# Kernel tuning notes

Hardware: AMD Instinct MI355X
Metric: run time of the kernel (lower is better)

Reference implementation:

```python
import jax, jax.numpy as jnp
import numpy as np

DIM = 1024
LN_EPS = 1e-5


def setup_inputs() -> dict:
    key = jax.random.key(0)
    ks = jax.random.split(key, 6)
    B, S, D = 8, 2048, DIM
    x = jax.random.normal(ks[0], (B, S, D), dtype=jnp.float32)
    mask = jnp.ones((B, S, 1), dtype=jnp.float32)
    # LayerNorm params
    ln_g = jnp.ones((D,), dtype=jnp.float32)
    ln_b = jnp.zeros((D,), dtype=jnp.float32)
    # FeedForward: Linear(D, D) -> GELU -> Linear(D, D); hidden_dim == dim per source
    lim = 1.0 / np.sqrt(D)
    w1 = jax.random.uniform(ks[1], (D, D), jnp.float32, -lim, lim)
    b1 = jax.random.uniform(ks[2], (D,), jnp.float32, -lim, lim)
    w2 = jax.random.uniform(ks[3], (D, D), jnp.float32, -lim, lim)
    b2 = jax.random.uniform(ks[4], (D,), jnp.float32, -lim, lim)
    return {"x": x, "mask": mask, "ln_g": ln_g, "ln_b": ln_b,
            "w1": w1, "b1": b1, "w2": w2, "b2": b2}


def _layernorm(t, g, b):
    mu = jnp.mean(t, axis=-1, keepdims=True)
    var = jnp.mean(jnp.square(t - mu), axis=-1, keepdims=True)
    return (t - mu) * jax.lax.rsqrt(var + LN_EPS) * g + b


def reference(x, mask, ln_g, ln_b, w1, b1, w2, b2):
    # torch.fft(t, signal_ndim=1): FFT over hidden axis (complex input, imag=0)
    ft = jnp.fft.fft(x.astype(jnp.float32), axis=-1)
    # torch.fft(., signal_ndim=2): 2D FFT over (seq, hidden)
    ft = jnp.fft.fft2(ft, axes=(-2, -1))
    ft = ft.real  # [..., 0] slice of the fake-complex tensor
    t = _layernorm(x + ft, ln_g, ln_b)
    # FeedForward: Linear -> GELU(exact) -> Linear (dropout is identity at eval)
    h = jax.nn.gelu(t @ w1 + b1, approximate=False)
    out = h @ w2 + b2
    return out * mask
```

## Files before the change

### kernel.cpp

```cpp
#include <hip/hip_runtime.h>
#include <math.h>

#define DIMD 1024
#define SEQ  2048
#define BATCH 8
#define ROWS (BATCH * SEQ)

#define MF 1152
#define KF 1088

typedef __attribute__((ext_vector_type(8))) short bf16x8;
typedef __attribute__((ext_vector_type(4))) float f32x4;
typedef __attribute__((ext_vector_type(16))) float f32x16;
typedef __attribute__((ext_vector_type(8))) unsigned short ushort8;

__device__ __forceinline__ unsigned short f2bf(float f) {
    unsigned u = __float_as_uint(f);
    unsigned r = (u + 0x7FFFu + ((u >> 16) & 1u)) >> 16;
    return (unsigned short)r;
}
__device__ __forceinline__ void gl_lds16(const void* g, void* l) {
    __builtin_amdgcn_global_load_lds(
        (const __attribute__((address_space(1))) unsigned int*)g,
        (__attribute__((address_space(3))) unsigned int*)l, 16, 0, 0);
}


__global__ __launch_bounds__(256) void build_acos(unsigned short* __restrict__ Acos) {
    int s = blockIdx.x;
    for (int t = threadIdx.x; t < KF; t += 256) {
        float c = 0.0f;
        if (t <= 1024) {
            int prod = (s * t) & (SEQ - 1);
            c = 1024.0f * cospif((float)prod * (1.0f / 1024.0f));
        }
        Acos[(size_t)s * KF + t] = f2bf(c);
    }
}

__global__ __launch_bounds__(256) void build_xe(const float* __restrict__ x,
                                                unsigned short* __restrict__ Xe) {
    int lane = threadIdx.x & 63;
    int oct  = threadIdx.x >> 6;
    int n = blockIdx.x * 64 + lane;
    int b = n >> 10, d = n & 1023;
    int rd = (DIMD - d) & (DIMD - 1);
    int t0 = blockIdx.y * 32 + oct * 8;
    const float* xb = x + (size_t)b * SEQ * DIMD + rd;
    ushort8 tmp;
    #pragma unroll
    for (int j = 0; j < 8; ++j) {
        int t = t0 + j;
        float v;
        if (t == 0)          v = xb[0];
        else if (t < 1024)   v = xb[(size_t)t * DIMD] + xb[(size_t)(2048 - t) * DIMD];
        else if (t == 1024)  v = xb[(size_t)1024 * DIMD];
        else                 v = 0.0f;
        tmp[j] = f2bf(v);
    }
    *(ushort8*)&Xe[(size_t)n * KF + t0] = tmp;
}

__global__ __launch_bounds__(256) void pack_wt(const float* __restrict__ W,
                                               unsigned short* __restrict__ Wt) {
    int lane = threadIdx.x & 63;
    int oct = threadIdx.x >> 6;
    int n = blockIdx.x * 64 + lane;
    int k0 = blockIdx.y * 32 + oct * 8;
    ushort8 tmp;
    #pragma unroll
    for (int j = 0; j < 8; ++j) tmp[j] = f2bf(W[(size_t)(k0 + j) * DIMD + n]);
    *(ushort8*)&Wt[(size_t)n * DIMD + k0] = tmp;
}

template <int MODE>
__global__ __launch_bounds__(256, 2) void gemm32(const unsigned short* __restrict__ A,
                                                 const unsigned short* __restrict__ B,
                                                 int K, int lda, int ldb, int ldc,
                                                 const float* __restrict__ bias,
                                                 const float* __restrict__ mask,
                                                 void* __restrict__ outp) {
    __shared__ unsigned short As[2][128 * 64];
    __shared__ unsigned short Bs[2][128 * 64];

    const int tid  = threadIdx.x;
    const int lane = tid & 63;
    const int w    = tid >> 6;
    const int wm   = w >> 1;
    const int wn   = w & 1;
    const int r31  = lane & 31;
    const int hl   = lane >> 5;
    const int sw   = lane & 7;

    const int st_row = lane >> 3;
    const int st_col = ((lane & 7) ^ st_row) * 8;

    int bx = blockIdx.x, by = blockIdx.y;
    if (MODE != 0) {
        int lin = bx + 8 * by;
        int c = lin & 7, r = lin >> 3;
        by = c * 16 + (r >> 3);
        bx = r & 7;
    }
    const int m0 = by * 128;
    const int n0 = bx * 128;

    const int rA = wm * 64 + r31;
    const int rB = wn * 64 + r31;

    auto stage = [&](int buf, int kt) {
        int kb = kt * 64 + st_col;
        #pragma unroll
        for (int c = 0; c < 4; ++c) {
            int ch = w + c * 4;
            gl_lds16(&A[(size_t)(m0 + ch * 8 + st_row) * lda + kb], &As[buf][ch * 512]);
            gl_lds16(&B[(size_t)(n0 + ch * 8 + st_row) * ldb + kb], &Bs[buf][ch * 512]);
        }
    };

    f32x16 acc[2][2] = {};
    bf16x8 a0[2], b0[2], a1[2], b1[2];

#define READK(SA, SB, PA, PB, KK)                                                    \
    {                                                                                \
        const int so_ = ((((KK) * 2) + hl) ^ sw) * 8;                                \
        _Pragma("unroll") for (int bi = 0; bi < 2; ++bi)                             \
            SA[bi] = *(const bf16x8*)&(PA)[(rA + bi * 32) * 64 + so_];               \
        _Pragma("unroll") for (int bj = 0; bj < 2; ++bj)                             \
            SB[bj] = *(const bf16x8*)&(PB)[(rB + bj * 32) * 64 + so_];               \
    }

#define MFMAK(SA, SB)                                                                \
    __builtin_amdgcn_s_setprio(1);                                                   \
    _Pragma("unroll") for (int bi = 0; bi < 2; ++bi)                                 \
        _Pragma("unroll") for (int bj = 0; bj < 2; ++bj)                             \
            acc[bi][bj] = __builtin_amdgcn_mfma_f32_32x32x16_bf16(                   \
                SA[bi], SB[bj], acc[bi][bj], 0, 0, 0);                               \
    __builtin_amdgcn_s_setprio(0);

    const int NT = K >> 6;

    stage(0, 0);
    asm volatile("s_waitcnt vmcnt(0)" ::: "memory");
    __builtin_amdgcn_s_barrier();

    int cur = 0;
    for (int t = 0; t < NT; ++t) {
        const unsigned short* pa = &As[cur][0];
        const unsigned short* pb = &Bs[cur][0];
        int nk = (t + 1 < NT) ? t + 1 : NT - 1;
        READK(a0, b0, pa, pb, 0)
        stage(cur ^ 1, nk);
        READK(a1, b1, pa, pb, 1)
        MFMAK(a0, b0)
        READK(a0, b0, pa, pb, 2)
        MFMAK(a1, b1)
        READK(a1, b1, pa, pb, 3)
        MFMAK(a0, b0)
        MFMAK(a1, b1)
        asm volatile("s_waitcnt vmcnt(0) lgkmcnt(0)" ::: "memory");
        __builtin_amdgcn_s_barrier();
        cur ^= 1;
    }
#undef MFMAK
#undef READK

    #pragma unroll
    for (int bi = 0; bi < 2; ++bi) {
        int rowb = m0 + wm * 64 + bi * 32 + 4 * hl;
        #pragma unroll
        for (int bj = 0; bj < 2; ++bj) {
            int col = n0 + wn * 64 + bj * 32 + r31;
            float bcol = (MODE != 0) ? bias[col] : 0.0f;
            #pragma unroll
            for (int r = 0; r < 16; ++r) {
                float v = acc[bi][bj][r];
                int row = rowb + (r & 3) + 8 * (r >> 2);
                if (MODE == 0) {
                    ((float*)outp)[(size_t)row * ldc + col] = v;
                } else if (MODE == 1) {
                    v += bcol;
                    v = 0.5f * v * (1.0f + erff(v * 0.70710678118654752f));
                    ((unsigned short*)outp)[(size_t)row * ldc + col] = f2bf(v);
                } else {
                    v += bcol;
                    v *= mask[row];
                    ((float*)outp)[(size_t)row * ldc + col] = v;
                }
            }
        }
    }
}

__global__ __launch_bounds__(256) void ln_pair(const float* __restrict__ x,
                                               const float* __restrict__ F,
                                               const float* __restrict__ g,
                                               const float* __restrict__ beta,
                                               unsigned short* __restrict__ t) {
    const int sp = blockIdx.x;
    const int b  = blockIdx.y;

    float4 fv = ((const float4*)(F + (size_t)sp * 8192 + (size_t)b * 1024))[threadIdx.x];
    float4 g4 = ((const float4*)g)[threadIdx.x];
    float4 b4 = ((const float4*)beta)[threadIdx.x];

    __shared__ float red[4];
    const int wave = threadIdx.x >> 6;
    const int lane = threadIdx.x & 63;

    const int nrows = (sp >= 1 && sp <= 1023) ? 2 : 1;
    for (int p = 0; p < nrows; ++p) {
        int s = p ? (2048 - sp) : sp;
        int row = b * SEQ + s;
        float4 xv = ((const float4*)(x + (size_t)row * DIMD))[threadIdx.x];
        float v0 = xv.x + fv.x, v1 = xv.y + fv.y, v2 = xv.z + fv.z, v3 = xv.w + fv.w;

        float sm = v0 + v1 + v2 + v3;
        #pragma unroll
        for (int off = 32; off > 0; off >>= 1) sm += __shfl_down(sm, off, 64);
        if (lane == 0) red[wave] = sm;
        __syncthreads();
        const float mean = (red[0] + red[1] + red[2] + red[3]) * (1.0f / DIMD);

        float dx0 = v0 - mean, dx1 = v1 - mean, dx2 = v2 - mean, dx3 = v3 - mean;
        float q = dx0 * dx0 + dx1 * dx1 + dx2 * dx2 + dx3 * dx3;
        __syncthreads();
        #pragma unroll
        for (int off = 32; off > 0; off >>= 1) q += __shfl_down(q, off, 64);
        if (lane == 0) red[wave] = q;
        __syncthreads();
        const float var = (red[0] + red[1] + red[2] + red[3]) * (1.0f / DIMD);
        const float rstd = rsqrtf(var + 1e-5f);

        ushort4 o;
        o.x = f2bf(dx0 * rstd * g4.x + b4.x);
        o.y = f2bf(dx1 * rstd * g4.y + b4.y);
        o.z = f2bf(dx2 * rstd * g4.z + b4.z);
        o.w = f2bf(dx3 * rstd * g4.w + b4.w);
        ((ushort4*)(t + (size_t)row * DIMD))[threadIdx.x] = o;
        __syncthreads();
    }
}

#define BM 64
#define BN 64
#define BK 16

__global__ __launch_bounds__(256) void fft_cos_kernel(const float* __restrict__ x,
                                                      float* __restrict__ y) {
    __shared__ float tab[SEQ];
    __shared__ float As[BM][BK + 1];
    __shared__ float Bs[BK][BN + 1];
    const int tid = threadIdx.x;
    const int b = blockIdx.z;
    const int s0 = blockIdx.y * BM;
    const int n0 = blockIdx.x * BN;
    for (int i = tid; i < SEQ; i += 256) tab[i] = cospif((float)i * (1.0f / 1024.0f));
    const int tx = tid & 15;
    const int ty = tid >> 4;
    float acc[4][4] = {};
    const float* Xb = x + (size_t)b * SEQ * DIMD;
    for (int k0 = 0; k0 < SEQ; k0 += BK) {
        __syncthreads();
        for (int f = tid; f < BM * BK; f += 256) {
            int i = f / BK, k = f % BK;
            int prod = (s0 + i) * (k0 + k);
            As[i][k] = tab[prod & (SEQ - 1)];
        }
        for (int f = tid; f < BK * BN; f += 256) {
            int k = f / BN, j = f % BN;
            int d = n0 + j;
            int rd = (DIMD - d) & (DIMD - 1);
            Bs[k][j] = Xb[(size_t)(k0 + k) * DIMD + rd];
        }
        __syncthreads();
        #pragma unroll
        for (int k = 0; k < BK; ++k) {
            float a[4], bv[4];
            #pragma unroll
            for (int i = 0; i < 4; ++i) a[i] = As[ty * 4 + i][k];
            #pragma unroll
            for (int j = 0; j < 4; ++j) bv[j] = Bs[k][tx * 4 + j];
            #pragma unroll
            for (int i = 0; i < 4; ++i)
                #pragma unroll
                for (int j = 0; j < 4; ++j) acc[i][j] += a[i] * bv[j];
        }
    }
    #pragma unroll
    for (int i = 0; i < 4; ++i) {
        int s = s0 + ty * 4 + i;
        #pragma unroll
        for (int j = 0; j < 4; ++j) {
            int d = n0 + tx * 4 + j;
            y[((size_t)b * SEQ + s) * DIMD + d] = Xb[(size_t)s * DIMD + d] + 1024.0f * acc[i][j];
        }
    }
}

__global__ __launch_bounds__(256) void ln_kernel(float* __restrict__ y,
                                                 const float* __restrict__ g,
                                                 const float* __restrict__ beta) {
    const int row = blockIdx.x;
    float4* p = (float4*)(y + (size_t)row * DIMD);
    float4 v = p[threadIdx.x];
    __shared__ float red[4];
    const int wave = threadIdx.x >> 6;
    const int lane = threadIdx.x & 63;
    float s = v.x + v.y + v.z + v.w;
    #pragma unroll
    for (int off = 32; off > 0; off >>= 1) s += __shfl_down(s, off, 64);
    if (lane == 0) red[wave] = s;
    __syncthreads();
    const float mean = (red[0] + red[1] + red[2] + red[3]) * (1.0f / DIMD);
    float dx0 = v.x - mean, dx1 = v.y - mean, dx2 = v.z - mean, dx3 = v.w - mean;
    float q = dx0 * dx0 + dx1 * dx1 + dx2 * dx2 + dx3 * dx3;
    __syncthreads();
    #pragma unroll
    for (int off = 32; off > 0; off >>= 1) q += __shfl_down(q, off, 64);
    if (lane == 0) red[wave] = q;
    __syncthreads();
    const float var = (red[0] + red[1] + red[2] + red[3]) * (1.0f / DIMD);
    const float rstd = rsqrtf(var + 1e-5f);
    float4 g4 = ((const float4*)g)[threadIdx.x];
    float4 b4 = ((const float4*)beta)[threadIdx.x];
    float4 o;
    o.x = dx0 * rstd * g4.x + b4.x;
    o.y = dx1 * rstd * g4.y + b4.y;
    o.z = dx2 * rstd * g4.z + b4.z;
    o.w = dx3 * rstd * g4.w + b4.w;
    p[threadIdx.x] = o;
}

template <int MODE>
__global__ __launch_bounds__(256) void ff_gemm(const float* __restrict__ A,
                                               const float* __restrict__ W,
                                               const float* __restrict__ bias,
                                               const float* __restrict__ mask,
                                               float* __restrict__ out) {
    __shared__ float As[BM][BK + 1];
    __shared__ float Bs[BK][BN + 1];
    const int tid = threadIdx.x;
    const int tx = tid & 15;
    const int ty = tid >> 4;
    const int m0 = blockIdx.y * BM;
    const int n0 = blockIdx.x * BN;
    float acc[4][4] = {};
    for (int k0 = 0; k0 < DIMD; k0 += BK) {
        __syncthreads();
        for (int f = tid; f < BM * BK; f += 256) {
            int i = f / BK, k = f % BK;
            As[i][k] = A[(size_t)(m0 + i) * DIMD + k0 + k];
        }
        for (int f = tid; f < BK * BN; f += 256) {
            int k = f / BN, j = f % BN;
            Bs[k][j] = W[(size_t)(k0 + k) * DIMD + n0 + j];
        }
        __syncthreads();
        #pragma unroll
        for (int k = 0; k < BK; ++k) {
            float a[4], bv[4];
            #pragma unroll
            for (int i = 0; i < 4; ++i) a[i] = As[ty * 4 + i][k];
            #pragma unroll
            for (int j = 0; j < 4; ++j) bv[j] = Bs[k][tx * 4 + j];
            #pragma unroll
            for (int i = 0; i < 4; ++i)
                #pragma unroll
                for (int j = 0; j < 4; ++j) acc[i][j] += a[i] * bv[j];
        }
    }
    #pragma unroll
    for (int i = 0; i < 4; ++i) {
        int m = m0 + ty * 4 + i;
        float mk = (MODE == 1) ? mask[m] : 1.0f;
        #pragma unroll
        for (int j = 0; j < 4; ++j) {
            int n = n0 + tx * 4 + j;
            float v = acc[i][j] + bias[n];
            if (MODE == 0) v = 0.5f * v * (1.0f + erff(v * 0.70710678118654752f));
            else v *= mk;
            out[(size_t)m * DIMD + n] = v;
        }
    }
}

extern "C" void kernel_launch(void* const* d_in, const int* in_sizes, int n_in,
                              void* d_out, int out_size, void* d_ws, size_t ws_size,
                              hipStream_t stream) {
    const float* x    = (const float*)d_in[0];
    const float* mask = (const float*)d_in[1];
    const float* ln_g = (const float*)d_in[2];
    const float* ln_b = (const float*)d_in[3];
    const float* w1   = (const float*)d_in[4];
    const float* b1   = (const float*)d_in[5];
    const float* w2   = (const float*)d_in[6];
    const float* b2   = (const float*)d_in[7];
    float* out = (float*)d_out;

    const size_t MB = 1024 * 1024;
    dim3 blk(256);

    if (ws_size >= 70 * MB) {
        char* w = (char*)d_ws;
        unsigned short* Acos = (unsigned short*)w;
        unsigned short* Xe   = (unsigned short*)(w + 4 * MB);
        unsigned short* t    = (unsigned short*)(w + 32 * MB);
        unsigned short* h    = (unsigned short*)w;
        unsigned short* W1t  = (unsigned short*)(w + 64 * MB);
        unsigned short* W2t  = (unsigned short*)(w + 66 * MB);
        float* F = (float*)d_out;

        build_acos<<<dim3(MF), blk, 0, stream>>>(Acos);
        build_xe<<<dim3(8192 / 64, KF / 32), blk, 0, stream>>>(x, Xe);
        pack_wt<<<dim3(1024 / 64, 1024 / 32), blk, 0, stream>>>(w1, W1t);
        pack_wt<<<dim3(1024 / 64, 1024 / 32), blk, 0, stream>>>(w2, W2t);

        gemm32<0><<<dim3(8192 / 128, MF / 128), blk, 0, stream>>>(
            Acos, Xe, KF, KF, KF, 8192, nullptr, nullptr, F);
        ln_pair<<<dim3(1025, BATCH), blk, 0, stream>>>(x, F, ln_g, ln_b, t);
        gemm32<1><<<dim3(1024 / 128, ROWS / 128), blk, 0, stream>>>(
            t, W1t, 1024, 1024, 1024, 1024, b1, nullptr, h);
        gemm32<2><<<dim3(1024 / 128, ROWS / 128), blk, 0, stream>>>(
            h, W2t, 1024, 1024, 1024, 1024, b2, mask, out);
    } else {
        float* yf = (float*)d_ws;
        const size_t bufBytes = (size_t)ROWS * DIMD * sizeof(float);
        fft_cos_kernel<<<dim3(DIMD / BN, SEQ / BM, BATCH), blk, 0, stream>>>(x, yf);
        ln_kernel<<<dim3(ROWS), blk, 0, stream>>>(yf, ln_g, ln_b);
        ff_gemm<0><<<dim3(DIMD / BN, ROWS / BM), blk, 0, stream>>>(yf, w1, b1, nullptr, out);
        ff_gemm<1><<<dim3(DIMD / BN, ROWS / BM), blk, 0, stream>>>(out, w2, b2, mask, yf);
        hipMemcpyAsync(d_out, yf, bufBytes, hipMemcpyDeviceToDevice, stream);
    }
}
```

Before: 317.9 us.

## Fuse prep kernels and switch GEMMs to 128x64 single-buffered tiles

```diff
diff --git a/kernel.cpp b/kernel.cpp
--- a/kernel.cpp
+++ b/kernel.cpp
@@ -10,7 +10,6 @@
 #define KF 1088
 
 typedef __attribute__((ext_vector_type(8))) short bf16x8;
-typedef __attribute__((ext_vector_type(4))) float f32x4;
 typedef __attribute__((ext_vector_type(16))) float f32x16;
 typedef __attribute__((ext_vector_type(8))) unsigned short ushort8;
 
@@ -25,152 +24,161 @@
         (__attribute__((address_space(3))) unsigned int*)l, 16, 0, 0);
 }
 
-
-__global__ __launch_bounds__(256) void build_acos(unsigned short* __restrict__ Acos) {
-    int s = blockIdx.x;
-    for (int t = threadIdx.x; t < KF; t += 256) {
-        float c = 0.0f;
-        if (t <= 1024) {
-            int prod = (s * t) & (SEQ - 1);
-            c = 1024.0f * cospif((float)prod * (1.0f / 1024.0f));
-        }
-        Acos[(size_t)s * KF + t] = f2bf(c);
-    }
-}
-
-__global__ __launch_bounds__(256) void build_xe(const float* __restrict__ x,
-                                                unsigned short* __restrict__ Xe) {
-    int lane = threadIdx.x & 63;
-    int oct  = threadIdx.x >> 6;
-    int n = blockIdx.x * 64 + lane;
-    int b = n >> 10, d = n & 1023;
-    int rd = (DIMD - d) & (DIMD - 1);
-    int t0 = blockIdx.y * 32 + oct * 8;
-    const float* xb = x + (size_t)b * SEQ * DIMD + rd;
-    ushort8 tmp;
-    #pragma unroll
-    for (int j = 0; j < 8; ++j) {
-        int t = t0 + j;
-        float v;
-        if (t == 0)          v = xb[0];
-        else if (t < 1024)   v = xb[(size_t)t * DIMD] + xb[(size_t)(2048 - t) * DIMD];
-        else if (t == 1024)  v = xb[(size_t)1024 * DIMD];
-        else                 v = 0.0f;
-        tmp[j] = f2bf(v);
-    }
-    *(ushort8*)&Xe[(size_t)n * KF + t0] = tmp;
-}
-
-__global__ __launch_bounds__(256) void pack_wt(const float* __restrict__ W,
-                                               unsigned short* __restrict__ Wt) {
-    int lane = threadIdx.x & 63;
-    int oct = threadIdx.x >> 6;
-    int n = blockIdx.x * 64 + lane;
-    int k0 = blockIdx.y * 32 + oct * 8;
-    ushort8 tmp;
-    #pragma unroll
-    for (int j = 0; j < 8; ++j) tmp[j] = f2bf(W[(size_t)(k0 + j) * DIMD + n]);
-    *(ushort8*)&Wt[(size_t)n * DIMD + k0] = tmp;
+__global__ __launch_bounds__(256) void build_all(const float* __restrict__ x,
+                                                 const float* __restrict__ w1,
+                                                 const float* __restrict__ w2,
+                                                 unsigned short* __restrict__ Acos,
+                                                 unsigned short* __restrict__ Xe,
+                                                 unsigned short* __restrict__ W1t,
+                                                 unsigned short* __restrict__ W2t) {
+    const int bid  = blockIdx.x;
+    const int lane = threadIdx.x & 63;
+    const int oct  = threadIdx.x >> 6;
+
+    if (bid < MF) {
+        int s = bid;
+        for (int t = threadIdx.x; t < KF; t += 256) {
+            float c = 0.0f;
+            if (t <= 1024) {
+                int prod = (s * t) & (SEQ - 1);
+                c = 1024.0f * cospif((float)prod * (1.0f / 1024.0f));
+            }
+            Acos[(size_t)s * KF + t] = f2bf(c);
+        }
+    } else if (bid < MF + 4352) {
+        int i = bid - MF;
+        int bx = i & 127;
+        int byy = i >> 7;
+        int n = bx * 64 + lane;
+        int b = n >> 10, d = n & 1023;
+        int rd = (DIMD - d) & (DIMD - 1);
+        int t0 = byy * 32 + oct * 8;
+        const float* xb = x + (size_t)b * SEQ * DIMD + rd;
+        ushort8 tmp;
+        #pragma unroll
+        for (int j = 0; j < 8; ++j) {
+            int t = t0 + j;
+            float v;
+            if (t == 0)          v = xb[0];
+            else if (t < 1024)   v = xb[(size_t)t * DIMD] + xb[(size_t)(2048 - t) * DIMD];
+            else if (t == 1024)  v = xb[(size_t)1024 * DIMD];
+            else                 v = 0.0f;
+            tmp[j] = f2bf(v);
+        }
+        *(ushort8*)&Xe[(size_t)n * KF + t0] = tmp;
+    } else {
+        int i = bid - (MF + 4352);
+        const float* W = (i < 512) ? w1 : w2;
+        unsigned short* Wt = (i < 512) ? W1t : W2t;
+        i &= 511;
+        int n = (i & 15) * 64 + lane;
+        int k0 = (i >> 4) * 32 + oct * 8;
+        ushort8 tmp;
+        #pragma unroll
+        for (int j = 0; j < 8; ++j) tmp[j] = f2bf(W[(size_t)(k0 + j) * DIMD + n]);
+        *(ushort8*)&Wt[(size_t)n * DIMD + k0] = tmp;
+    }
 }
 
 template <int MODE>
-__global__ __launch_bounds__(256, 2) void gemm32(const unsigned short* __restrict__ A,
-                                                 const unsigned short* __restrict__ B,
-                                                 int K, int lda, int ldb, int ldc,
-                                                 const float* __restrict__ bias,
-                                                 const float* __restrict__ mask,
-                                                 void* __restrict__ outp) {
-    __shared__ unsigned short As[2][128 * 64];
-    __shared__ unsigned short Bs[2][128 * 64];
+__global__ __launch_bounds__(128) void gemmsw(const unsigned short* __restrict__ A,
+                                              const unsigned short* __restrict__ B,
+                                              int K, int lda, int ldb, int ldc,
+                                              const float* __restrict__ bias,
+                                              const float* __restrict__ mask,
+                                              void* __restrict__ outp) {
+    __shared__ unsigned short As[16 * 520];
+    __shared__ unsigned short Bs[8 * 520];
 
     const int tid  = threadIdx.x;
     const int lane = tid & 63;
     const int w    = tid >> 6;
-    const int wm   = w >> 1;
-    const int wn   = w & 1;
     const int r31  = lane & 31;
     const int hl   = lane >> 5;
-    const int sw   = lane & 7;
-
-    const int st_row = lane >> 3;
-    const int st_col = ((lane & 7) ^ st_row) * 8;
+    const int st_row  = lane >> 3;
+    const int st_slot = lane & 7;
 
     int bx = blockIdx.x, by = blockIdx.y;
-    if (MODE != 0) {
-        int lin = bx + 8 * by;
-        int c = lin & 7, r = lin >> 3;
-        by = c * 16 + (r >> 3);
-        bx = r & 7;
+    {
+        int gx = gridDim.x;
+        int nwg = gx * gridDim.y;
+        int lin = bx + gx * by;
+        int cpx = nwg >> 3;
+        int g = (lin & 7) * cpx + (lin >> 3);
+        by = g / gx;
+        bx = g - by * gx;
     }
     const int m0 = by * 128;
-    const int n0 = bx * 128;
-
-    const int rA = wm * 64 + r31;
-    const int rB = wn * 64 + r31;
-
-    auto stage = [&](int buf, int kt) {
-        int kb = kt * 64 + st_col;
-        #pragma unroll
-        for (int c = 0; c < 4; ++c) {
-            int ch = w + c * 4;
-            gl_lds16(&A[(size_t)(m0 + ch * 8 + st_row) * lda + kb], &As[buf][ch * 512]);
-            gl_lds16(&B[(size_t)(n0 + ch * 8 + st_row) * ldb + kb], &Bs[buf][ch * 512]);
+    const int n0 = bx * 64;
+
+    auto stage = [&](int kt) {
+        int kb = kt * 64;
+        #pragma unroll
+        for (int i = 0; i < 8; ++i) {
+            int ch = w * 8 + i;
+            int g = (st_slot - ch) & 7;
+            gl_lds16(&A[(size_t)(m0 + ch * 8 + st_row) * lda + kb + g * 8],
+                     &As[ch * 520]);
+        }
+        #pragma unroll
+        for (int i = 0; i < 4; ++i) {
+            int ch = w * 4 + i;
+            int g = (st_slot - ch) & 7;
+            gl_lds16(&B[(size_t)(n0 + ch * 8 + st_row) * ldb + kb + g * 8],
+                     &Bs[ch * 520]);
         }
     };
 
     f32x16 acc[2][2] = {};
     bf16x8 a0[2], b0[2], a1[2], b1[2];
 
-#define READK(SA, SB, PA, PB, KK)                                                    \
+#define READK(SA, SB, KK)                                                            \
     {                                                                                \
-        const int so_ = ((((KK) * 2) + hl) ^ sw) * 8;                                \
-        _Pragma("unroll") for (int bi = 0; bi < 2; ++bi)                             \
-            SA[bi] = *(const bf16x8*)&(PA)[(rA + bi * 32) * 64 + so_];               \
-        _Pragma("unroll") for (int bj = 0; bj < 2; ++bj)                             \
-            SB[bj] = *(const bf16x8*)&(PB)[(rB + bj * 32) * 64 + so_];               \
+        const int g_ = (KK) * 2 + hl;                                                \
+        _Pragma("unroll") for (int bi = 0; bi < 2; ++bi) {                           \
+            int r_ = w * 64 + bi * 32 + r31;                                         \
+            int C_ = r_ >> 3;                                                        \
+            SA[bi] = *(const bf16x8*)&As[C_ * 520 + (r_ & 7) * 64                    \
+                                         + ((g_ + C_) & 7) * 8];                     \
+        }                                                                            \
+        _Pragma("unroll") for (int bj = 0; bj < 2; ++bj) {                           \
+            int r_ = bj * 32 + r31;                                                  \
+            int C_ = r_ >> 3;                                                        \
+            SB[bj] = *(const bf16x8*)&Bs[C_ * 520 + (r_ & 7) * 64                    \
+                                         + ((g_ + C_) & 7) * 8];                     \
+        }                                                                            \
     }
 
 #define MFMAK(SA, SB)                                                                \
-    __builtin_amdgcn_s_setprio(1);                                                   \
     _Pragma("unroll") for (int bi = 0; bi < 2; ++bi)                                 \
         _Pragma("unroll") for (int bj = 0; bj < 2; ++bj)                             \
             acc[bi][bj] = __builtin_amdgcn_mfma_f32_32x32x16_bf16(                   \
-                SA[bi], SB[bj], acc[bi][bj], 0, 0, 0);                               \
-    __builtin_amdgcn_s_setprio(0);
+                SA[bi], SB[bj], acc[bi][bj], 0, 0, 0);
 
     const int NT = K >> 6;
 
-    stage(0, 0);
-    asm volatile("s_waitcnt vmcnt(0)" ::: "memory");
-    __builtin_amdgcn_s_barrier();
-
-    int cur = 0;
-    for (int t = 0; t < NT; ++t) {
-        const unsigned short* pa = &As[cur][0];
-        const unsigned short* pb = &Bs[cur][0];
-        int nk = (t + 1 < NT) ? t + 1 : NT - 1;
-        READK(a0, b0, pa, pb, 0)
-        stage(cur ^ 1, nk);
-        READK(a1, b1, pa, pb, 1)
+    for (int kt = 0; kt < NT; ++kt) {
+        __syncthreads();
+        stage(kt);
+        __syncthreads();
+        READK(a0, b0, 0)
+        READK(a1, b1, 1)
         MFMAK(a0, b0)
-        READK(a0, b0, pa, pb, 2)
+        READK(a0, b0, 2)
         MFMAK(a1, b1)
-        READK(a1, b1, pa, pb, 3)
+        READK(a1, b1, 3)
         MFMAK(a0, b0)
         MFMAK(a1, b1)
-        asm volatile("s_waitcnt vmcnt(0) lgkmcnt(0)" ::: "memory");
-        __builtin_amdgcn_s_barrier();
-        cur ^= 1;
     }
 #undef MFMAK
 #undef READK
 
     #pragma unroll
     for (int bi = 0; bi < 2; ++bi) {
-        int rowb = m0 + wm * 64 + bi * 32 + 4 * hl;
+        int rowb = m0 + w * 64 + bi * 32 + 4 * hl;
         #pragma unroll
         for (int bj = 0; bj < 2; ++bj) {
-            int col = n0 + wn * 64 + bj * 32 + r31;
+            int col = n0 + bj * 32 + r31;
             float bcol = (MODE != 0) ? bias[col] : 0.0f;
             #pragma unroll
             for (int r = 0; r < 16; ++r) {
@@ -400,6 +408,7 @@
 
     const size_t MB = 1024 * 1024;
     dim3 blk(256);
+    dim3 blk128(128);
 
     if (ws_size >= 70 * MB) {
         char* w = (char*)d_ws;
@@ -411,17 +420,15 @@
         unsigned short* W2t  = (unsigned short*)(w + 66 * MB);
         float* F = (float*)d_out;
 
-        build_acos<<<dim3(MF), blk, 0, stream>>>(Acos);
-        build_xe<<<dim3(8192 / 64, KF / 32), blk, 0, stream>>>(x, Xe);
-        pack_wt<<<dim3(1024 / 64, 1024 / 32), blk, 0, stream>>>(w1, W1t);
-        pack_wt<<<dim3(1024 / 64, 1024 / 32), blk, 0, stream>>>(w2, W2t);
-
-        gemm32<0><<<dim3(8192 / 128, MF / 128), blk, 0, stream>>>(
+        build_all<<<dim3(MF + 4352 + 1024), blk, 0, stream>>>(
+            x, w1, w2, Acos, Xe, W1t, W2t);
+
+        gemmsw<0><<<dim3(8192 / 64, MF / 128), blk128, 0, stream>>>(
             Acos, Xe, KF, KF, KF, 8192, nullptr, nullptr, F);
         ln_pair<<<dim3(1025, BATCH), blk, 0, stream>>>(x, F, ln_g, ln_b, t);
-        gemm32<1><<<dim3(1024 / 128, ROWS / 128), blk, 0, stream>>>(
+        gemmsw<1><<<dim3(1024 / 64, ROWS / 128), blk128, 0, stream>>>(
             t, W1t, 1024, 1024, 1024, 1024, b1, nullptr, h);
-        gemm32<2><<<dim3(1024 / 128, ROWS / 128), blk, 0, stream>>>(
+        gemmsw<2><<<dim3(1024 / 64, ROWS / 128), blk128, 0, stream>>>(
             h, W2t, 1024, 1024, 1024, 1024, b2, mask, out);
     } else {
         float* yf = (float*)d_ws;
```

After: 318.6 us. About the same (+0.2%).
